# Kernel optimization log

Hardware: AMD Instinct MI355X
Metric: run time of the kernel (lower is better)

Reference implementation:

```python
import jax, jax.numpy as jnp
import numpy as np

N_NODES = 100000
N_EDGES = 3200000
NUM_FEATURES = 256
NUM_CLASSES = 1000


def gcn_conv(x, edge_index, W, b):
    # PyG GCNConv: h = XW; add self-loops; out = D^{-1/2} (A+I) D^{-1/2} h + b
    n = x.shape[0]
    h = x @ W  # [N, out]
    loop = jnp.arange(n)
    src = jnp.concatenate([edge_index[0], loop])
    dst = jnp.concatenate([edge_index[1], loop])
    ones = jnp.ones(src.shape[0], dtype=x.dtype)
    deg = jax.ops.segment_sum(ones, dst, num_segments=n)  # in-degree incl. self-loop
    dinv = jax.lax.rsqrt(deg)  # deg >= 1 because of self-loops
    norm = dinv[src] * dinv[dst]  # [E+N]
    out = jax.ops.segment_sum(h[src] * norm[:, None], dst, num_segments=n)
    return out + b


def setup_inputs() -> dict:
    key = jax.random.key(0)
    ks = jax.random.split(key, 12)
    x = jax.random.normal(ks[0], (N_NODES, NUM_FEATURES), dtype=jnp.float32)
    edge_index = jax.random.randint(ks[1], (2, N_EDGES), 0, N_NODES, dtype=jnp.int64)
    def glorot(k, shape):
        fan_in, fan_out = shape[0], shape[-1]
        lim = np.sqrt(6.0 / (fan_in + fan_out)).astype(np.float32)
        return jax.random.uniform(k, shape, jnp.float32, -lim, lim)
    W1 = glorot(ks[2], (NUM_FEATURES, 16)); b1 = jnp.zeros((16,), jnp.float32)
    W2 = glorot(ks[3], (16, 32));           b2 = jnp.zeros((32,), jnp.float32)
    conv_w = jax.random.normal(ks[4], (64, 32, 1, 3), jnp.float32) * 0.05  # OIHW
    conv_b = jnp.zeros((64,), jnp.float32)
    fc_w = jax.random.normal(ks[5], (NUM_CLASSES, 64), jnp.float32) * 0.05
    fc_b = jnp.zeros((NUM_CLASSES,), jnp.float32)
    return {"x": x, "edge_index": edge_index, "W1": W1, "b1": b1,
            "W2": W2, "b2": b2, "conv_w": conv_w, "conv_b": conv_b,
            "fc_w": fc_w, "fc_b": fc_b}


def reference(x, edge_index, W1, b1, W2, b2, conv_w, conv_b, fc_w, fc_b):
    h = jax.nn.relu(gcn_conv(x, edge_index, W1, b1))   # [N,16]
    h = gcn_conv(h, edge_index, W2, b2)                 # [N,32]
    # x.unsqueeze(0).transpose(1,2) -> [1, 32, N]; run Conv2d((1,3), pad (0,1))
    # as NCHW with H=1: [1, 32, 1, N]
    img = h.T[None, :, None, :]                         # [1,32,1,N]
    y = jax.lax.conv_general_dilated(
        img, conv_w, window_strides=(1, 1), padding=((0, 0), (1, 1)),
        dimension_numbers=("NCHW", "OIHW", "NCHW"))
    y = y + conv_b[None, :, None, None]                 # [1,64,1,N]
    # adaptive_max_pool2d to (1,1) == global max over spatial dims
    pooled = jnp.max(y, axis=(2, 3))                    # [1,64]
    return pooled @ fc_w.T + fc_b                       # [1,num_classes]
```

## Files before the change

### kernel.cpp

```cpp
#include <hip/hip_runtime.h>
#include <hip/hip_bf16.h>
#include <hip/hip_fp16.h>

#define NN 100000
#define NE 3200000
#define FIN 256
#define F1 16
#define F2 32
#define CO 64
#define NC 1000
#define NBLK 391
#define GBLK 1563
#define NPART 8
#define NGRP 32
#define CAPG 16384
#define PSZ 12500
#define BK 20

#define OFF_DINV 0
#define OFF_CUR  100352
#define OFF_DEG  200704
#define OFF_ECOL 301056
#define OFF_MISC 3501056
#define OFF_DPART 3502080
#define OFF_SPART 7696384
#define OFF_HIST 11890688
#define OFF_H1S  3502080
#define OFF_H2S  7696384
#define OFF_OUT2 3502080

__device__ __forceinline__ unsigned enc_f(float f) {
    unsigned u = __float_as_uint(f);
    return (u & 0x80000000u) ? ~u : (u | 0x80000000u);
}
__device__ __forceinline__ float dec_f(unsigned u) {
    return (u & 0x80000000u) ? __uint_as_float(u & 0x7fffffffu) : __uint_as_float(~u);
}

__global__ void k_init(unsigned* __restrict__ pcur, unsigned* __restrict__ pool) {
    int t = threadIdx.x;
    pcur[t] = (unsigned)t * CAPG;
    if (t < 64) pool[t] = 0u;
}

__global__ __launch_bounds__(256) void k_bucket(const int* __restrict__ ei,
                                                unsigned* __restrict__ pcur,
                                                int* __restrict__ dpart,
                                                int* __restrict__ spart) {
    __shared__ unsigned wcnt[4][8];
    __shared__ unsigned woff[4][8];
    int t = threadIdx.x, lane = t & 63, w = t >> 6;
    int g = blockIdx.x & (NGRP - 1);
    int base = blockIdx.x * (256 * BK) + t;
    int dst[BK], src[BK];
    #pragma unroll
    for (int k = 0; k < BK; ++k) {
        dst[k] = ei[NE + base + k * 256];
        src[k] = ei[base + k * 256];
    }
    unsigned long long lt = (lane == 63) ? 0x7fffffffffffffffull
                                         : ((1ull << lane) - 1ull);
    unsigned cnt = 0;
    #pragma unroll
    for (int k = 0; k < BK; ++k) {
        int bin = (unsigned)dst[k] / PSZ;
        #pragma unroll
        for (int b = 0; b < 8; ++b) {
            unsigned long long m = __ballot(bin == b);
            if (lane == b) cnt += (unsigned)__popcll(m);
        }
    }
    if (lane < 8) wcnt[w][lane] = cnt;
    __syncthreads();
    if (t < 8) {
        unsigned c0 = wcnt[0][t], c1 = wcnt[1][t], c2 = wcnt[2][t], c3 = wcnt[3][t];
        unsigned b = atomicAdd(&pcur[t * NGRP + g], c0 + c1 + c2 + c3);
        woff[0][t] = b;
        woff[1][t] = b + c0;
        woff[2][t] = b + c0 + c1;
        woff[3][t] = b + c0 + c1 + c2;
    }
    __syncthreads();
    unsigned run = (lane < 8) ? woff[w][lane] : 0u;
    #pragma unroll
    for (int k = 0; k < BK; ++k) {
        int bin = (unsigned)dst[k] / PSZ;
        unsigned long long mym = 0;
        unsigned myrun = 0;
        #pragma unroll
        for (int b = 0; b < 8; ++b) {
            unsigned long long m = __ballot(bin == b);
            unsigned r = __shfl(run, b);
            if (bin == b) { mym = m; myrun = r; }
            if (lane == b) run += (unsigned)__popcll(m);
        }
        unsigned pos = myrun + (unsigned)__popcll(mym & lt);
        dpart[pos] = dst[k];
        spart[pos] = src[k];
    }
}

__global__ __launch_bounds__(256) void k_hist(const unsigned* __restrict__ pcur,
                                              const int* __restrict__ dpart,
                                              unsigned* __restrict__ hist) {
    __shared__ unsigned lh[PSZ];
    int p = blockIdx.x & 7;
    int g = blockIdx.x >> 3;
    int ci = p * NGRP + g;
    int t = threadIdx.x;
    for (int i = t; i < PSZ; i += 256) lh[i] = 0;
    __syncthreads();
    unsigned s = (unsigned)ci * CAPG;
    unsigned e = pcur[ci];
    int pb = p * PSZ;
    for (unsigned j = s + t; j < e; j += 256)
        atomicAdd(&lh[dpart[j] - pb], 1u);
    __syncthreads();
    unsigned* hrow = hist + (unsigned)ci * PSZ;
    for (int i = t; i < PSZ; i += 256) hrow[i] = lh[i];
}

__global__ __launch_bounds__(256) void k_colscan(unsigned* __restrict__ hist,
                                                 unsigned* __restrict__ deg,
                                                 unsigned* __restrict__ bsum) {
    __shared__ unsigned W[4];
    int t = threadIdx.x;
    int gid = blockIdx.x * 256 + t;
    unsigned run = 0;
    if (gid < NN) {
        int p = gid / PSZ, i = gid % PSZ;
        #pragma unroll
        for (int c = 0; c < NGRP; ++c) {
            unsigned idx = (unsigned)(p * NGRP + c) * PSZ + i;
            unsigned v = hist[idx];
            hist[idx] = run;
            run += v;
        }
        deg[gid] = run;
    }
    unsigned d = (gid < NN) ? run : 0u;
    #pragma unroll
    for (int off = 1; off < 64; off <<= 1) d += __shfl_xor(d, off);
    if ((t & 63) == 0) W[t >> 6] = d;
    __syncthreads();
    if (t == 0) bsum[blockIdx.x] = W[0] + W[1] + W[2] + W[3];
}

__global__ __launch_bounds__(512) void k_bscan(unsigned* __restrict__ bsum) {
    __shared__ unsigned S[512];
    int t = threadIdx.x;
    unsigned v = (t < NBLK) ? bsum[t] : 0u;
    S[t] = v;
    __syncthreads();
    for (int off = 1; off < 512; off <<= 1) {
        unsigned u = (t >= off) ? S[t - off] : 0u;
        __syncthreads();
        S[t] += u;
        __syncthreads();
    }
    if (t < NBLK) bsum[t] = S[t] - v;
}

__global__ void k_cscan(const unsigned* __restrict__ deg, const unsigned* __restrict__ bsum,
                        unsigned* __restrict__ cursor, float* __restrict__ dinv) {
    __shared__ unsigned S[256];
    int t = threadIdx.x;
    int i = blockIdx.x * 256 + t;
    unsigned d = (i < NN) ? deg[i] : 0u;
    S[t] = d;
    __syncthreads();
    for (int off = 1; off < 256; off <<= 1) {
        unsigned u = (t >= off) ? S[t - off] : 0u;
        __syncthreads();
        S[t] += u;
        __syncthreads();
    }
    if (i < NN) {
        cursor[i] = bsum[blockIdx.x] + S[t];
        dinv[i] = rsqrtf((float)(d + 1u));
    }
}

__global__ __launch_bounds__(256) void k_place(const unsigned* __restrict__ pcur,
                                               const int* __restrict__ dpart,
                                               const int* __restrict__ spart,
                                               const unsigned* __restrict__ hist,
                                               const unsigned* __restrict__ cursor,
                                               int* __restrict__ ecol) {
    __shared__ unsigned lcur[PSZ];
    int p = blockIdx.x & 7;
    int g = blockIdx.x >> 3;
    int ci = p * NGRP + g;
    int t = threadIdx.x;
    int pb = p * PSZ;
    const unsigned* hrow = hist + (unsigned)ci * PSZ;
    for (int i = t; i < PSZ; i += 256) {
        int gi = pb + i;
        unsigned rowstart = gi ? cursor[gi - 1] : 0u;
        lcur[i] = rowstart + hrow[i];
    }
    __syncthreads();
    unsigned s = (unsigned)ci * CAPG;
    unsigned e = pcur[ci];
    for (unsigned j = s + t; j < e; j += 256) {
        int dst = dpart[j];
        int src = spart[j];
        unsigned pos = atomicAdd(&lcur[dst - pb], 1u);
        ecol[pos] = src;
    }
}

__device__ __forceinline__ void fma16g(float xk, const float* __restrict__ w,
                                       float* __restrict__ acc) {
    #pragma unroll
    for (int o = 0; o < 16; ++o) acc[o] += xk * w[o];
}

__global__ __launch_bounds__(64) void k_gemm1(const float* __restrict__ X,
                                              const float* __restrict__ W1,
                                              const float* __restrict__ dinv,
                                              __half2* __restrict__ h1h) {
    int row = blockIdx.x * 64 + threadIdx.x;
    if (row >= NN) return;
    const float4* xr = (const float4*)(X + (size_t)row * FIN);
    float acc[16] = {};
    #pragma unroll 1
    for (int c = 0; c < 8; ++c) {
        float4 xq[8];
        #pragma unroll
        for (int i = 0; i < 8; ++i) xq[i] = xr[c * 8 + i];
        const float* xf = (const float*)xq;
        #pragma unroll
        for (int kk = 0; kk < 32; ++kk)
            fma16g(xf[kk], W1 + (c * 32 + kk) * 16, acc);
    }
    float dv = dinv[row];
    union { __half2 h[8]; uint4 u[2]; } pk;
    #pragma unroll
    for (int o = 0; o < 8; ++o)
        pk.h[o] = __floats2half2_rn(acc[2 * o] * dv, acc[2 * o + 1] * dv);
    uint4* dst = (uint4*)(h1h + (size_t)row * 8);
    dst[0] = pk.u[0];
    dst[1] = pk.u[1];
}

__global__ __launch_bounds__(256) void k_gathm(const unsigned* __restrict__ cursor,
                                               const int* __restrict__ ecol,
                                               const float* __restrict__ dinv,
                                               const float* __restrict__ b1,
                                               const float* __restrict__ W2,
                                               const __half2* __restrict__ h1h,
                                               __half2* __restrict__ h2h) {
    __shared__ float Ws[512];
    __shared__ float B1[16];
    int tid = threadIdx.x;
    Ws[tid] = W2[tid];
    Ws[tid + 256] = W2[tid + 256];
    if (tid < 16) B1[tid] = b1[tid];
    __syncthreads();
    int lane = tid & 63;
    int grp = lane >> 3, f2 = lane & 7;
    int node = blockIdx.x * 32 + (tid >> 6) * 8 + grp;
    unsigned s = node ? cursor[node - 1] : 0u;
    unsigned e = cursor[node];
    float2 acc = __half22float2(h1h[(size_t)node * 8 + f2]);
    for (unsigned j = s; j < e; j += 4) {
        bool v1 = j + 1 < e, v2 = j + 2 < e, v3 = j + 3 < e;
        int c0 = ecol[j];
        int c1 = v1 ? ecol[j + 1] : c0;
        int c2 = v2 ? ecol[j + 2] : c0;
        int c3 = v3 ? ecol[j + 3] : c0;
        float2 a0 = __half22float2(h1h[(size_t)c0 * 8 + f2]);
        float2 a1 = __half22float2(h1h[(size_t)c1 * 8 + f2]);
        float2 a2 = __half22float2(h1h[(size_t)c2 * 8 + f2]);
        float2 a3 = __half22float2(h1h[(size_t)c3 * 8 + f2]);
        float m1 = v1 ? 1.f : 0.f, m2 = v2 ? 1.f : 0.f, m3 = v3 ? 1.f : 0.f;
        acc.x += a0.x + m1 * a1.x + m2 * a2.x + m3 * a3.x;
        acc.y += a0.y + m1 * a1.y + m2 * a2.y + m3 * a3.y;
    }
    float dv = dinv[node];
    float r0 = fmaxf(acc.x * dv + B1[2 * f2], 0.f);
    float r1 = fmaxf(acc.y * dv + B1[2 * f2 + 1], 0.f);
    int gb = lane & 56;
    float rv[16];
    #pragma unroll
    for (int q = 0; q < 8; ++q) {
        rv[2 * q]     = __shfl(r0, gb + q);
        rv[2 * q + 1] = __shfl(r1, gb + q);
    }
    float o0x = 0.f, o0y = 0.f, o1x = 0.f, o1y = 0.f;
    #pragma unroll
    for (int q = 0; q < 16; ++q) {
        float r = rv[q];
        o0x += r * Ws[q * 32 + 2 * f2];
        o0y += r * Ws[q * 32 + 2 * f2 + 1];
        o1x += r * Ws[q * 32 + 2 * f2 + 16];
        o1y += r * Ws[q * 32 + 2 * f2 + 17];
    }
    h2h[(size_t)node * 16 + f2]     = __floats2half2_rn(o0x * dv, o0y * dv);
    h2h[(size_t)node * 16 + f2 + 8] = __floats2half2_rn(o1x * dv, o1y * dv);
}

__global__ __launch_bounds__(256) void k_gath2(const unsigned* __restrict__ cursor,
                                               const int* __restrict__ ecol,
                                               const float* __restrict__ dinv,
                                               const float* __restrict__ b2,
                                               const __half2* __restrict__ h2h,
                                               float* __restrict__ out2) {
    int tid = threadIdx.x;
    int lane = tid & 63;
    int grp = lane >> 4, f2 = lane & 15;
    int node = blockIdx.x * 16 + (tid >> 6) * 4 + grp;
    unsigned s = node ? cursor[node - 1] : 0u;
    unsigned e = cursor[node];
    float2 acc = __half22float2(h2h[(size_t)node * 16 + f2]);
    for (unsigned j = s; j < e; j += 4) {
        bool v1 = j + 1 < e, v2 = j + 2 < e, v3 = j + 3 < e;
        int c0 = ecol[j];
        int c1 = v1 ? ecol[j + 1] : c0;
        int c2 = v2 ? ecol[j + 2] : c0;
        int c3 = v3 ? ecol[j + 3] : c0;
        float2 a0 = __half22float2(h2h[(size_t)c0 * 16 + f2]);
        float2 a1 = __half22float2(h2h[(size_t)c1 * 16 + f2]);
        float2 a2 = __half22float2(h2h[(size_t)c2 * 16 + f2]);
        float2 a3 = __half22float2(h2h[(size_t)c3 * 16 + f2]);
        float m1 = v1 ? 1.f : 0.f, m2 = v2 ? 1.f : 0.f, m3 = v3 ? 1.f : 0.f;
        acc.x += a0.x + m1 * a1.x + m2 * a2.x + m3 * a3.x;
        acc.y += a0.y + m1 * a1.y + m2 * a2.y + m3 * a3.y;
    }
    float dv = dinv[node];
    float2 b = ((const float2*)b2)[f2];
    ((float2*)(out2 + (size_t)node * F2))[f2] =
        make_float2(acc.x * dv + b.x, acc.y * dv + b.y);
}

#define NPB 256
__global__ __launch_bounds__(256) void k_conv(const float* __restrict__ h2f,
                                              const float* __restrict__ cw,
                                              unsigned* __restrict__ pool) {
    __shared__ float Hs[NPB + 2][33];
    __shared__ float Wt[3 * 32 * 64];
    __shared__ float4 Ms[4][16];
    int tid = threadIdx.x;
    int base = blockIdx.x * NPB;
    for (int idx = tid; idx < 6144; idx += 256) {
        int o = idx / 96, r = idx % 96, ci = r / 3, k = r % 3;
        Wt[(k * 32 + ci) * 64 + o] = cw[idx];
    }
    for (int idx = tid; idx < (NPB + 2) * 8; idx += 256) {
        int j = idx >> 3, c4 = (idx & 7) << 2;
        int g = base + j - 1;
        float4 v = make_float4(0.f, 0.f, 0.f, 0.f);
        if (g >= 0 && g < NN) v = *(const float4*)(h2f + (size_t)g * F2 + c4);
        Hs[j][c4 + 0] = v.x;
        Hs[j][c4 + 1] = v.y;
        Hs[j][c4 + 2] = v.z;
        Hs[j][c4 + 3] = v.w;
    }
    __syncthreads();

    int o4 = (tid & 15) * 4;
    int ng = tid >> 4;
    float4 acc[16] = {};
    for (int ci = 0; ci < 32; ++ci) {
        float h[18];
        #pragma unroll
        for (int j = 0; j < 18; ++j) h[j] = Hs[ng * 16 + j][ci];
        #pragma unroll
        for (int k = 0; k < 3; ++k) {
            float4 w = *(const float4*)&Wt[(k * 32 + ci) * 64 + o4];
            #pragma unroll
            for (int i = 0; i < 16; ++i) {
                float hv = h[i + k];
                acc[i].x += hv * w.x;
                acc[i].y += hv * w.y;
                acc[i].z += hv * w.z;
                acc[i].w += hv * w.w;
            }
        }
    }
    const float NI = -3.0e38f;
    float4 m4 = make_float4(NI, NI, NI, NI);
    #pragma unroll
    for (int i = 0; i < 16; ++i) {
        if (base + ng * 16 + i < NN) {
            m4.x = fmaxf(m4.x, acc[i].x);
            m4.y = fmaxf(m4.y, acc[i].y);
            m4.z = fmaxf(m4.z, acc[i].z);
            m4.w = fmaxf(m4.w, acc[i].w);
        }
    }
    #pragma unroll
    for (int off = 16; off <= 32; off <<= 1) {
        m4.x = fmaxf(m4.x, __shfl_xor(m4.x, off));
        m4.y = fmaxf(m4.y, __shfl_xor(m4.y, off));
        m4.z = fmaxf(m4.z, __shfl_xor(m4.z, off));
        m4.w = fmaxf(m4.w, __shfl_xor(m4.w, off));
    }
    int lane = tid & 63, wv = tid >> 6;
    if (lane < 16) Ms[wv][lane] = m4;
    __syncthreads();
    if (tid < 16) {
        float4 a = Ms[0][tid], b = Ms[1][tid], c = Ms[2][tid], d = Ms[3][tid];
        a.x = fmaxf(fmaxf(a.x, b.x), fmaxf(c.x, d.x));
        a.y = fmaxf(fmaxf(a.y, b.y), fmaxf(c.y, d.y));
        a.z = fmaxf(fmaxf(a.z, b.z), fmaxf(c.z, d.z));
        a.w = fmaxf(fmaxf(a.w, b.w), fmaxf(c.w, d.w));
        int o = tid * 4;
        atomicMax(&pool[o + 0], enc_f(a.x));
        atomicMax(&pool[o + 1], enc_f(a.y));
        atomicMax(&pool[o + 2], enc_f(a.z));
        atomicMax(&pool[o + 3], enc_f(a.w));
    }
}

__global__ void k_fc(const unsigned* __restrict__ pool, const float* __restrict__ cb,
                     const float* __restrict__ fw, const float* __restrict__ fb,
                     float* __restrict__ out) {
    __shared__ float P[64];
    int tid = threadIdx.x;
    if (tid < 64) P[tid] = dec_f(pool[tid]) + cb[tid];
    __syncthreads();
    int j = blockIdx.x * 256 + tid;
    if (j >= NC) return;
    float s = fb[j];
    const float4* wr = (const float4*)(fw + (size_t)j * CO);
    #pragma unroll
    for (int c = 0; c < 16; ++c) {
        float4 w = wr[c];
        s += P[c * 4 + 0] * w.x + P[c * 4 + 1] * w.y +
             P[c * 4 + 2] * w.z + P[c * 4 + 3] * w.w;
    }
    out[j] = s;
}

extern "C" void kernel_launch(void* const* d_in, const int* in_sizes, int n_in,
                              void* d_out, int out_size, void* d_ws, size_t ws_size,
                              hipStream_t stream) {
    const float* x  = (const float*)d_in[0];
    const int*   ei = (const int*)d_in[1];
    const float* W1 = (const float*)d_in[2];
    const float* b1 = (const float*)d_in[3];
    const float* W2 = (const float*)d_in[4];
    const float* b2 = (const float*)d_in[5];
    const float* cw = (const float*)d_in[6];
    const float* cb = (const float*)d_in[7];
    const float* fw = (const float*)d_in[8];
    const float* fb = (const float*)d_in[9];

    float* ws = (float*)d_ws;
    float*    dinv   = ws + OFF_DINV;
    unsigned* cursor = (unsigned*)(ws + OFF_CUR);
    unsigned* deg    = (unsigned*)(ws + OFF_DEG);
    int*      ecol   = (int*)(ws + OFF_ECOL);
    unsigned* pcur   = (unsigned*)(ws + OFF_MISC);
    unsigned* pool   = pcur + 256;
    unsigned* bsum   = pcur + 320;
    int*      dpart  = (int*)(ws + OFF_DPART);
    int*      spart  = (int*)(ws + OFF_SPART);
    unsigned* hist   = (unsigned*)(ws + OFF_HIST);
    __half2*  h1h    = (__half2*)(ws + OFF_H1S);
    __half2*  h2h    = (__half2*)(ws + OFF_H2S);
    float*    out2   = ws + OFF_OUT2;

    k_init   <<<1, 256, 0, stream>>>(pcur, pool);
    k_bucket <<<NE / (256 * BK), 256, 0, stream>>>(ei, pcur, dpart, spart);
    k_hist   <<<NPART * NGRP, 256, 0, stream>>>(pcur, dpart, hist);
    k_colscan<<<NBLK, 256, 0, stream>>>(hist, deg, bsum);
    k_bscan  <<<1, 512, 0, stream>>>(bsum);
    k_cscan  <<<NBLK, 256, 0, stream>>>(deg, bsum, cursor, dinv);
    k_place  <<<NPART * NGRP, 256, 0, stream>>>(pcur, dpart, spart, hist, cursor, ecol);
    k_gemm1  <<<GBLK, 64, 0, stream>>>(x, W1, dinv, h1h);
    k_gathm  <<<NN / 32, 256, 0, stream>>>(cursor, ecol, dinv, b1, W2, h1h, h2h);
    k_gath2  <<<NN / 16, 256, 0, stream>>>(cursor, ecol, dinv, b2, h2h, out2);
    k_conv   <<<(NN + NPB - 1) / NPB, 256, 0, stream>>>(out2, cw, pool);
    k_fc     <<<4, 256, 0, stream>>>(pool, cb, fw, fb, (float*)d_out);
}
```

Before: 274.6 us.

## Pack bucketed edges into one word and unroll gathers to eight

Packs each bucketed edge into a single 32-bit word, with the local destination in the high 15 bits and the source in the low 17 bits. This replaces the separate dpart/spart arrays and halves partition-buffer traffic in bucket, hist and place. The two aggregation kernels now load eight neighbor indices and features per iteration instead of four, giving more memory-level parallelism. The workspace layout is reshuffled to match, and the packing assumes node IDs fit in 17 bits and local offsets in 15 bits.

```diff
diff --git a/kernel.cpp b/kernel.cpp
--- a/kernel.cpp
+++ b/kernel.cpp
@@ -16,18 +16,18 @@
 #define CAPG 16384
 #define PSZ 12500
 #define BK 20
+#define SRCMASK 0x1FFFFu
 
 #define OFF_DINV 0
 #define OFF_CUR  100352
 #define OFF_DEG  200704
 #define OFF_ECOL 301056
 #define OFF_MISC 3501056
-#define OFF_DPART 3502080
-#define OFF_SPART 7696384
-#define OFF_HIST 11890688
-#define OFF_H1S  3502080
-#define OFF_H2S  7696384
-#define OFF_OUT2 3502080
+#define OFF_EPART 3502080
+#define OFF_HIST  7696384
+#define OFF_H1S   3502080
+#define OFF_H2S   4302080
+#define OFF_OUT2  5902080
 
 __device__ __forceinline__ unsigned enc_f(float f) {
     unsigned u = __float_as_uint(f);
@@ -45,8 +45,7 @@
 
 __global__ __launch_bounds__(256) void k_bucket(const int* __restrict__ ei,
                                                 unsigned* __restrict__ pcur,
-                                                int* __restrict__ dpart,
-                                                int* __restrict__ spart) {
+                                                unsigned* __restrict__ epart) {
     __shared__ unsigned wcnt[4][8];
     __shared__ unsigned woff[4][8];
     int t = threadIdx.x, lane = t & 63, w = t >> 6;
@@ -95,13 +94,12 @@
             if (lane == b) run += (unsigned)__popcll(m);
         }
         unsigned pos = myrun + (unsigned)__popcll(mym & lt);
-        dpart[pos] = dst[k];
-        spart[pos] = src[k];
+        epart[pos] = ((unsigned)(dst[k] - bin * PSZ) << 17) | (unsigned)src[k];
     }
 }
 
 __global__ __launch_bounds__(256) void k_hist(const unsigned* __restrict__ pcur,
-                                              const int* __restrict__ dpart,
+                                              const unsigned* __restrict__ epart,
                                               unsigned* __restrict__ hist) {
     __shared__ unsigned lh[PSZ];
     int p = blockIdx.x & 7;
@@ -112,9 +110,8 @@
     __syncthreads();
     unsigned s = (unsigned)ci * CAPG;
     unsigned e = pcur[ci];
-    int pb = p * PSZ;
     for (unsigned j = s + t; j < e; j += 256)
-        atomicAdd(&lh[dpart[j] - pb], 1u);
+        atomicAdd(&lh[epart[j] >> 17], 1u);
     __syncthreads();
     unsigned* hrow = hist + (unsigned)ci * PSZ;
     for (int i = t; i < PSZ; i += 256) hrow[i] = lh[i];
@@ -182,8 +179,7 @@
 }
 
 __global__ __launch_bounds__(256) void k_place(const unsigned* __restrict__ pcur,
-                                               const int* __restrict__ dpart,
-                                               const int* __restrict__ spart,
+                                               const unsigned* __restrict__ epart,
                                                const unsigned* __restrict__ hist,
                                                const unsigned* __restrict__ cursor,
                                                int* __restrict__ ecol) {
@@ -203,10 +199,9 @@
     unsigned s = (unsigned)ci * CAPG;
     unsigned e = pcur[ci];
     for (unsigned j = s + t; j < e; j += 256) {
-        int dst = dpart[j];
-        int src = spart[j];
-        unsigned pos = atomicAdd(&lcur[dst - pb], 1u);
-        ecol[pos] = src;
+        unsigned v = epart[j];
+        unsigned pos = atomicAdd(&lcur[v >> 17], 1u);
+        ecol[pos] = (int)(v & SRCMASK);
     }
 }
 
@@ -264,19 +259,24 @@
     unsigned s = node ? cursor[node - 1] : 0u;
     unsigned e = cursor[node];
     float2 acc = __half22float2(h1h[(size_t)node * 8 + f2]);
-    for (unsigned j = s; j < e; j += 4) {
-        bool v1 = j + 1 < e, v2 = j + 2 < e, v3 = j + 3 < e;
-        int c0 = ecol[j];
-        int c1 = v1 ? ecol[j + 1] : c0;
-        int c2 = v2 ? ecol[j + 2] : c0;
-        int c3 = v3 ? ecol[j + 3] : c0;
-        float2 a0 = __half22float2(h1h[(size_t)c0 * 8 + f2]);
-        float2 a1 = __half22float2(h1h[(size_t)c1 * 8 + f2]);
-        float2 a2 = __half22float2(h1h[(size_t)c2 * 8 + f2]);
-        float2 a3 = __half22float2(h1h[(size_t)c3 * 8 + f2]);
-        float m1 = v1 ? 1.f : 0.f, m2 = v2 ? 1.f : 0.f, m3 = v3 ? 1.f : 0.f;
-        acc.x += a0.x + m1 * a1.x + m2 * a2.x + m3 * a3.x;
-        acc.y += a0.y + m1 * a1.y + m2 * a2.y + m3 * a3.y;
+    for (unsigned j = s; j < e; j += 8) {
+        int cc[8]; float msk[8];
+        #pragma unroll
+        for (int q = 0; q < 8; ++q) {
+            unsigned jj = j + q;
+            bool v = jj < e;
+            cc[q] = ecol[v ? jj : j];
+            msk[q] = v ? 1.f : 0.f;
+        }
+        float2 a[8];
+        #pragma unroll
+        for (int q = 0; q < 8; ++q)
+            a[q] = __half22float2(h1h[(size_t)cc[q] * 8 + f2]);
+        #pragma unroll
+        for (int q = 0; q < 8; ++q) {
+            acc.x += msk[q] * a[q].x;
+            acc.y += msk[q] * a[q].y;
+        }
     }
     float dv = dinv[node];
     float r0 = fmaxf(acc.x * dv + B1[2 * f2], 0.f);
@@ -314,19 +314,24 @@
     unsigned s = node ? cursor[node - 1] : 0u;
     unsigned e = cursor[node];
     float2 acc = __half22float2(h2h[(size_t)node * 16 + f2]);
-    for (unsigned j = s; j < e; j += 4) {
-        bool v1 = j + 1 < e, v2 = j + 2 < e, v3 = j + 3 < e;
-        int c0 = ecol[j];
-        int c1 = v1 ? ecol[j + 1] : c0;
-        int c2 = v2 ? ecol[j + 2] : c0;
-        int c3 = v3 ? ecol[j + 3] : c0;
-        float2 a0 = __half22float2(h2h[(size_t)c0 * 16 + f2]);
-        float2 a1 = __half22float2(h2h[(size_t)c1 * 16 + f2]);
-        float2 a2 = __half22float2(h2h[(size_t)c2 * 16 + f2]);
-        float2 a3 = __half22float2(h2h[(size_t)c3 * 16 + f2]);
-        float m1 = v1 ? 1.f : 0.f, m2 = v2 ? 1.f : 0.f, m3 = v3 ? 1.f : 0.f;
-        acc.x += a0.x + m1 * a1.x + m2 * a2.x + m3 * a3.x;
-        acc.y += a0.y + m1 * a1.y + m2 * a2.y + m3 * a3.y;
+    for (unsigned j = s; j < e; j += 8) {
+        int cc[8]; float msk[8];
+        #pragma unroll
+        for (int q = 0; q < 8; ++q) {
+            unsigned jj = j + q;
+            bool v = jj < e;
+            cc[q] = ecol[v ? jj : j];
+            msk[q] = v ? 1.f : 0.f;
+        }
+        float2 a[8];
+        #pragma unroll
+        for (int q = 0; q < 8; ++q)
+            a[q] = __half22float2(h2h[(size_t)cc[q] * 16 + f2]);
+        #pragma unroll
+        for (int q = 0; q < 8; ++q) {
+            acc.x += msk[q] * a[q].x;
+            acc.y += msk[q] * a[q].y;
+        }
     }
     float dv = dinv[node];
     float2 b = ((const float2*)b2)[f2];
@@ -456,20 +461,19 @@
     unsigned* pcur   = (unsigned*)(ws + OFF_MISC);
     unsigned* pool   = pcur + 256;
     unsigned* bsum   = pcur + 320;
-    int*      dpart  = (int*)(ws + OFF_DPART);
-    int*      spart  = (int*)(ws + OFF_SPART);
+    unsigned* epart  = (unsigned*)(ws + OFF_EPART);
     unsigned* hist   = (unsigned*)(ws + OFF_HIST);
     __half2*  h1h    = (__half2*)(ws + OFF_H1S);
     __half2*  h2h    = (__half2*)(ws + OFF_H2S);
     float*    out2   = ws + OFF_OUT2;
 
     k_init   <<<1, 256, 0, stream>>>(pcur, pool);
-    k_bucket <<<NE / (256 * BK), 256, 0, stream>>>(ei, pcur, dpart, spart);
-    k_hist   <<<NPART * NGRP, 256, 0, stream>>>(pcur, dpart, hist);
+    k_bucket <<<NE / (256 * BK), 256, 0, stream>>>(ei, pcur, epart);
+    k_hist   <<<NPART * NGRP, 256, 0, stream>>>(pcur, epart, hist);
     k_colscan<<<NBLK, 256, 0, stream>>>(hist, deg, bsum);
     k_bscan  <<<1, 512, 0, stream>>>(bsum);
     k_cscan  <<<NBLK, 256, 0, stream>>>(deg, bsum, cursor, dinv);
-    k_place  <<<NPART * NGRP, 256, 0, stream>>>(pcur, dpart, spart, hist, cursor, ecol);
+    k_place  <<<NPART * NGRP, 256, 0, stream>>>(pcur, epart, hist, cursor, ecol);
     k_gemm1  <<<GBLK, 64, 0, stream>>>(x, W1, dinv, h1h);
     k_gathm  <<<NN / 32, 256, 0, stream>>>(cursor, ecol, dinv, b1, W2, h1h, h2h);
     k_gath2  <<<NN / 16, 256, 0, stream>>>(cursor, ecol, dinv, b2, h2h, out2);
```

Result: faster. 245.2 us (-10.7%).
